# Performance work log

Hardware: AMD Instinct MI355X
Metric: run time of the kernel (lower is better)

The kernel has to match this reference:

```python
import jax, jax.numpy as jnp
import numpy as np

CONTEXT_SIZE = 32
NDIM = 64
HEAD_SIZE = 64
BATCH = 16384


def setup_inputs() -> dict:
    key = jax.random.key(0)
    kx, kk, kq, kv = jax.random.split(key, 4)
    x = jax.random.normal(kx, (BATCH, CONTEXT_SIZE, NDIM), dtype=jnp.float32)
    # nn.Linear(ndim, head_size, bias=False): y = x @ W.T, W is [head_size, ndim].
    # We store transposed weights [ndim, head_size] so y = x @ W.
    scale = 1.0 / np.sqrt(NDIM)
    Wk = jax.random.normal(kk, (NDIM, HEAD_SIZE), dtype=jnp.float32) * scale
    Wq = jax.random.normal(kq, (NDIM, HEAD_SIZE), dtype=jnp.float32) * scale
    Wv = jax.random.normal(kv, (NDIM, HEAD_SIZE), dtype=jnp.float32) * scale
    return {"x": x, "Wk": Wk, "Wq": Wq, "Wv": Wv}


def reference(x, Wk, Wq, Wv):
    # x: [B, T, D] with T == CONTEXT_SIZE
    k = x @ Wk  # [B, T, H]
    q = x @ Wq  # [B, T, H]
    v = x @ Wv  # [B, T, H]
    # Faithful to source: p = q @ k^T / head_size**(-0.5) == q @ k^T * sqrt(head_size)
    p = jnp.einsum("bth,bsh->bts", q, k) * jnp.sqrt(jnp.float32(HEAD_SIZE))
    causal = jnp.tril(jnp.ones((CONTEXT_SIZE, CONTEXT_SIZE), dtype=bool))
    p = jnp.where(causal, p, -jnp.inf)
    p = jax.nn.softmax(p, axis=-1)
    # dropout is identity in eval mode
    return jnp.einsum("bts,bsh->bth", p, v)  # [B, T, H]
```

## Files before the change

### kernel.cpp

```cpp
#include <hip/hip_runtime.h>

typedef __attribute__((ext_vector_type(8))) short short8;
typedef __attribute__((ext_vector_type(4))) float f32x4;
typedef __attribute__((ext_vector_type(2))) unsigned int u32x2;

#define CTX 32
#define ND  64
#define NH  64
#define LOG2E_8 11.541560327111707f

#define OFF_MH 0
#define OFF_ML 8192
#define OFF_WAVE 16384
#define PWSTR 80
#define PW_RTH 0
#define PW_RTL 2560
#define PW_VT  0
#define PW_P   5120
#define WAVE_BYTES 7168
#define NREG 8
#define LDS_BYTES (OFF_WAVE + NREG * WAVE_BYTES)

__device__ __forceinline__ unsigned short f2bf(float f) {
  unsigned int u = __builtin_bit_cast(unsigned int, f);
  u += 0x7FFFu + ((u >> 16) & 1u);
  return (unsigned short)(u >> 16);
}
__device__ __forceinline__ float bf2f(unsigned short b) {
  unsigned int u = ((unsigned int)b) << 16;
  return __builtin_bit_cast(float, u);
}
__device__ __forceinline__ unsigned int pk2(float a, float b) {
  return (unsigned int)f2bf(a) | ((unsigned int)f2bf(b) << 16);
}

#define MFMA(a, b, c) __builtin_amdgcn_mfma_f32_16x16x32_bf16((a), (b), (c), 0, 0, 0)

__global__ __launch_bounds__(256) void mk_m(
    const float* __restrict__ Wq, const float* __restrict__ Wk,
    const float* __restrict__ Wv,
    unsigned short* __restrict__ MtH, unsigned short* __restrict__ MtL,
    unsigned short* __restrict__ WvT)
{
  const int idx = blockIdx.x * 256 + threadIdx.x;
  const int dp = idx >> 6, d = idx & 63;
  const float* wq = Wq + d * 64;
  const float* wk = Wk + dp * 64;
  float acc = 0.f;
  #pragma unroll
  for (int h = 0; h < 64; ++h) acc = fmaf(wq[h], wk[h], acc);
  acc *= LOG2E_8;
  const unsigned short hi = f2bf(acc);
  MtH[idx] = hi;
  MtL[idx] = f2bf(acc - bf2f(hi));
  WvT[idx] = f2bf(Wv[d * 64 + dp]);
}

struct Batch {
  short8 xh[2][2], xl[2][2];
  f32x4  pa[2][2];
  char*  wl;
  float* ob;
};

__device__ __forceinline__ void load_x(const float* __restrict__ xb,
                                       f32x4 (&xr)[2][2][2], int c, int g) {
  #pragma unroll
  for (int mt = 0; mt < 2; ++mt)
    #pragma unroll
    for (int kt = 0; kt < 2; ++kt) {
      const float* p = xb + (16 * mt + c) * ND + 32 * kt + 8 * g;
      xr[mt][kt][0] = *(const f32x4*)(p);
      xr[mt][kt][1] = *(const f32x4*)(p + 4);
    }
}

__device__ __forceinline__ void split_x(Batch& s, const f32x4 (&xr)[2][2][2]) {
  #pragma unroll
  for (int mt = 0; mt < 2; ++mt)
    #pragma unroll
    for (int kt = 0; kt < 2; ++kt) {
      short8 hi, lo;
      #pragma unroll
      for (int half = 0; half < 2; ++half)
        #pragma unroll
        for (int j = 0; j < 4; ++j) {
          const float f = xr[mt][kt][half][j];
          const unsigned short h = f2bf(f);
          hi[4 * half + j] = (short)h;
          lo[4 * half + j] = (short)f2bf(f - bf2f(h));
        }
      s.xh[mt][kt] = hi;
      s.xl[mt][kt] = lo;
    }
  #pragma unroll
  for (int i = 0; i < 2; ++i)
    #pragma unroll
    for (int j = 0; j < 2; ++j) s.pa[i][j] = f32x4{0.f, 0.f, 0.f, 0.f};
}

__device__ __forceinline__ void qk_fill(Batch& s, const char* lds,
                                        int kt, int ntl, int c, int g) {
  const int nt = 2 * kt + ntl;
  f32x4 a0 = {0.f, 0.f, 0.f, 0.f};
  f32x4 a1 = {0.f, 0.f, 0.f, 0.f};
  #pragma unroll
  for (int kk = 0; kk < 2; ++kk) {
    const int row = 16 * nt + c;
    const int byte = row * 128 + ((64 * kk + 16 * g) ^ ((row & 7) << 4));
    const short8 bh = *(const short8*)(lds + OFF_MH + byte);
    const short8 bl = *(const short8*)(lds + OFF_ML + byte);
    a0 = MFMA(s.xh[0][kk], bh, a0);
    a0 = MFMA(s.xh[0][kk], bl, a0);
    a0 = MFMA(s.xl[0][kk], bh, a0);
    a1 = MFMA(s.xh[1][kk], bh, a1);
    a1 = MFMA(s.xh[1][kk], bl, a1);
    a1 = MFMA(s.xl[1][kk], bh, a1);
  }
  #pragma unroll
  for (int j = 0; j < 4; ++j) {
    const int col2 = 2 * (16 * ntl + c);
    const int off0 = (4 * g + j) * PWSTR + col2;
    const int off1 = (16 + 4 * g + j) * PWSTR + col2;
    const unsigned short h0 = f2bf(a0[j]);
    *(unsigned short*)(s.wl + PW_RTH + off0) = h0;
    *(unsigned short*)(s.wl + PW_RTL + off0) = f2bf(a0[j] - bf2f(h0));
    const unsigned short h1 = f2bf(a1[j]);
    *(unsigned short*)(s.wl + PW_RTH + off1) = h1;
    *(unsigned short*)(s.wl + PW_RTL + off1) = f2bf(a1[j] - bf2f(h1));
  }
}

__device__ __forceinline__ void qk_consume(Batch& s, int kt, int c, int g) {
  short8 tH[2], tL[2];
  #pragma unroll
  for (int i = 0; i < 2; ++i) {
    const int off = (16 * i + c) * PWSTR + 16 * g;
    tH[i] = *(const short8*)(s.wl + PW_RTH + off);
    tL[i] = *(const short8*)(s.wl + PW_RTL + off);
  }
  #pragma unroll
  for (int mt = 0; mt < 2; ++mt)
    #pragma unroll
    for (int nt2 = 0; nt2 < 2; ++nt2) {
      s.pa[mt][nt2] = MFMA(s.xh[mt][kt], tH[nt2], s.pa[mt][nt2]);
      s.pa[mt][nt2] = MFMA(s.xl[mt][kt], tH[nt2], s.pa[mt][nt2]);
      s.pa[mt][nt2] = MFMA(s.xh[mt][kt], tL[nt2], s.pa[mt][nt2]);
    }
}

__device__ __forceinline__ void softmax_store(Batch& s, int c, int g) {
  char* const pbuf = s.wl + PW_P;
  #pragma unroll
  for (int nt = 0; nt < 2; ++nt) {
    const int t = 16 * nt + c;
    float v[8];
    #pragma unroll
    for (int mt = 0; mt < 2; ++mt)
      #pragma unroll
      for (int j = 0; j < 4; ++j) {
        const int sidx = 16 * mt + 4 * g + j;
        v[4 * mt + j] = (sidx <= t) ? s.pa[mt][nt][j] : -__builtin_inff();
      }
    float m = fmaxf(fmaxf(fmaxf(v[0], v[1]), fmaxf(v[2], v[3])),
                    fmaxf(fmaxf(v[4], v[5]), fmaxf(v[6], v[7])));
    m = fmaxf(m, __shfl_xor(m, 16));
    m = fmaxf(m, __shfl_xor(m, 32));
    float e[8], ssum = 0.f;
    #pragma unroll
    for (int i = 0; i < 8; ++i) { e[i] = exp2f(v[i] - m); ssum += e[i]; }
    ssum += __shfl_xor(ssum, 16);
    ssum += __shfl_xor(ssum, 32);
    const float r = __builtin_amdgcn_rcpf(ssum);
    #pragma unroll
    for (int mt = 0; mt < 2; ++mt) {
      const u32x2 w2 = {pk2(e[4 * mt] * r, e[4 * mt + 1] * r),
                        pk2(e[4 * mt + 2] * r, e[4 * mt + 3] * r)};
      *(u32x2*)(pbuf + t * 64 + 32 * mt + 8 * g) = w2;
    }
  }
}

__device__ __forceinline__ void vproj(Batch& s, const short8 (&bvr)[4][2],
                                      int c, int g) {
  #pragma unroll
  for (int nt = 0; nt < 4; ++nt) {
    f32x4 a0 = {0.f, 0.f, 0.f, 0.f};
    f32x4 a1 = {0.f, 0.f, 0.f, 0.f};
    #pragma unroll
    for (int kk = 0; kk < 2; ++kk) {
      a0 = MFMA(s.xh[0][kk], bvr[nt][kk], a0);
      a1 = MFMA(s.xh[1][kk], bvr[nt][kk], a1);
    }
    char* const vrow = s.wl + PW_VT + (16 * nt + c) * PWSTR;
    const u32x2 w0 = {pk2(a0[0], a0[1]), pk2(a0[2], a0[3])};
    const u32x2 w1 = {pk2(a1[0], a1[1]), pk2(a1[2], a1[3])};
    *(u32x2*)(vrow + 8 * g)      = w0;
    *(u32x2*)(vrow + 32 + 8 * g) = w1;
  }
}

__device__ __forceinline__ void pv_store(Batch& s, int c, int g) {
  char* const pbuf = s.wl + PW_P;
  const short8 ap0 = *(const short8*)(pbuf + c * 64 + 16 * g);
  const short8 ap1 = *(const short8*)(pbuf + (16 + c) * 64 + 16 * g);
  #pragma unroll
  for (int mh = 0; mh < 4; ++mh) {
    const short8 bv = *(const short8*)(s.wl + PW_VT + (16 * mh + c) * PWSTR + 16 * g);
    f32x4 o0 = {0.f, 0.f, 0.f, 0.f};
    f32x4 o1 = {0.f, 0.f, 0.f, 0.f};
    o0 = MFMA(bv, ap0, o0);
    o1 = MFMA(bv, ap1, o1);
    *(f32x4*)(s.ob + c * NH + 16 * mh + 4 * g)        = o0;
    *(f32x4*)(s.ob + (16 + c) * NH + 16 * mh + 4 * g) = o1;
  }
}

__global__ __launch_bounds__(256, 2) void head_fused(
    const float* __restrict__ x,
    const unsigned short* __restrict__ MtH, const unsigned short* __restrict__ MtL,
    const unsigned short* __restrict__ WvT,
    float* __restrict__ out)
{
  __shared__ __align__(16) char lds[LDS_BYTES];
  const int tid = threadIdx.x;

  {
    const unsigned int* srcH = (const unsigned int*)MtH;
    const unsigned int* srcL = (const unsigned int*)MtL;
    #pragma unroll
    for (int i = 0; i < 8; ++i) {
      const int e = tid + 256 * i;
      const int row = e >> 5;
      const int byte = row * 128 + (((e & 31) * 4) ^ ((row & 7) << 4));
      *(unsigned int*)(lds + OFF_MH + byte) = srcH[e];
      *(unsigned int*)(lds + OFF_ML + byte) = srcL[e];
    }
  }
  __syncthreads();

  const int wid  = tid >> 6;
  const int lane = tid & 63;
  const int c = lane & 15;
  const int g = lane >> 4;

  short8 bvr[4][2];
  #pragma unroll
  for (int nt = 0; nt < 4; ++nt)
    #pragma unroll
    for (int kk = 0; kk < 2; ++kk)
      bvr[nt][kk] = *(const short8*)(WvT + (16 * nt + c) * 64 + 32 * kk + 8 * g);

  const int w = blockIdx.x * 4 + wid;
  const long bA = 2L * w, bB = 2L * w + 1;

  Batch A, B;
  A.wl = lds + OFF_WAVE + (wid * 2 + 0) * WAVE_BYTES;
  B.wl = lds + OFF_WAVE + (wid * 2 + 1) * WAVE_BYTES;
  A.ob = out + bA * (CTX * NH);
  B.ob = out + bB * (CTX * NH);

  f32x4 xrA[2][2][2], xrB[2][2][2];
  load_x(x + bA * (CTX * ND), xrA, c, g);
  load_x(x + bB * (CTX * ND), xrB, c, g);

  split_x(A, xrA);
  split_x(B, xrB);

  #pragma unroll
  for (int kt = 0; kt < 2; ++kt) {
    qk_fill(A, lds, kt, 0, c, g);
    qk_fill(B, lds, kt, 0, c, g);
    qk_fill(A, lds, kt, 1, c, g);
    qk_fill(B, lds, kt, 1, c, g);
    qk_consume(A, kt, c, g);
    qk_consume(B, kt, c, g);
  }
  softmax_store(A, c, g);
  softmax_store(B, c, g);
  vproj(A, bvr, c, g);
  vproj(B, bvr, c, g);
  pv_store(A, c, g);
  pv_store(B, c, g);
}

extern "C" void kernel_launch(void* const* d_in, const int* in_sizes, int n_in,
                              void* d_out, int out_size, void* d_ws, size_t ws_size,
                              hipStream_t stream) {
  const float* x  = (const float*)d_in[0];
  const float* Wk = (const float*)d_in[1];
  const float* Wq = (const float*)d_in[2];
  const float* Wv = (const float*)d_in[3];
  float* out = (float*)d_out;

  unsigned short* MtH = (unsigned short*)d_ws;
  unsigned short* MtL = MtH + 64 * 64;
  unsigned short* WvT = MtL + 64 * 64;

  mk_m<<<dim3(16), dim3(256), 0, stream>>>(Wq, Wk, Wv, MtH, MtL, WvT);

  const int batch = in_sizes[0] / (CTX * ND);
  const int nwg = batch / 8;
  head_fused<<<dim3(nwg), dim3(256), 0, stream>>>(x, MtH, MtL, WvT, out);
}
```

Before: 64.26 us.

## Process batches sequentially per wave with prefetch, packed bf16 conversion, higher occupancy

Each wave now handles its two batches one after another, using a single LDS region, instead of interleaving two batches. The next batch's x is prefetched into registers while the current one is computed. The smaller per-block LDS footprint lets launch bounds ask for three blocks per SIMD. Scalar bf16 rounding is replaced with packed float2-to-bfloat162 conversions, and the P buffer now uses a padded stride. The trade is less instruction-level parallelism from interleaving, in exchange for better occupancy, load latency hiding and cheaper conversions.

Result: faster. 59.64 us (-7.2%).

```diff
diff --git a/kernel.cpp b/kernel.cpp
--- a/kernel.cpp
+++ b/kernel.cpp
@@ -1,13 +1,16 @@
 #include <hip/hip_runtime.h>
+#include <hip/hip_bf16.h>
 
 typedef __attribute__((ext_vector_type(8))) short short8;
 typedef __attribute__((ext_vector_type(4))) float f32x4;
 typedef __attribute__((ext_vector_type(2))) unsigned int u32x2;
+typedef __attribute__((ext_vector_type(4))) unsigned int u32x4;
 
 #define CTX 32
 #define ND  64
 #define NH  64
 #define LOG2E_8 11.541560327111707f
+#define NB_PER_WAVE 2
 
 #define OFF_MH 0
 #define OFF_ML 8192
@@ -17,9 +20,8 @@
 #define PW_RTL 2560
 #define PW_VT  0
 #define PW_P   5120
-#define WAVE_BYTES 7168
-#define NREG 8
-#define LDS_BYTES (OFF_WAVE + NREG * WAVE_BYTES)
+#define WAVE_BYTES 7680
+#define LDS_BYTES (OFF_WAVE + 4 * WAVE_BYTES)
 
 __device__ __forceinline__ unsigned short f2bf(float f) {
   unsigned int u = __builtin_bit_cast(unsigned int, f);
@@ -30,8 +32,16 @@
   unsigned int u = ((unsigned int)b) << 16;
   return __builtin_bit_cast(float, u);
 }
-__device__ __forceinline__ unsigned int pk2(float a, float b) {
-  return (unsigned int)f2bf(a) | ((unsigned int)f2bf(b) << 16);
+__device__ __forceinline__ unsigned int pkrn(float a, float b) {
+  const __hip_bfloat162 t = __float22bfloat162_rn(make_float2(a, b));
+  unsigned int u;
+  __builtin_memcpy(&u, &t, 4);
+  return u;
+}
+__device__ __forceinline__ float2 unpk(unsigned int w) {
+  __hip_bfloat162 t;
+  __builtin_memcpy(&t, &w, 4);
+  return __bfloat1622float2(t);
 }
 
 #define MFMA(a, b, c) __builtin_amdgcn_mfma_f32_16x16x32_bf16((a), (b), (c), 0, 0, 0)
@@ -75,24 +85,36 @@
     }
 }
 
+__device__ __forceinline__ void split8(const f32x4 a0, const f32x4 a1,
+                                       short8& hi, short8& lo) {
+  u32x4 hw, lw;
+  #pragma unroll
+  for (int w = 0; w < 2; ++w) {
+    {
+      const float x0 = a0[2 * w], x1 = a0[2 * w + 1];
+      const unsigned int h = pkrn(x0, x1);
+      const float2 hf = unpk(h);
+      hw[w] = h;
+      lw[w] = pkrn(x0 - hf.x, x1 - hf.y);
+    }
+    {
+      const float x0 = a1[2 * w], x1 = a1[2 * w + 1];
+      const unsigned int h = pkrn(x0, x1);
+      const float2 hf = unpk(h);
+      hw[2 + w] = h;
+      lw[2 + w] = pkrn(x0 - hf.x, x1 - hf.y);
+    }
+  }
+  hi = __builtin_bit_cast(short8, hw);
+  lo = __builtin_bit_cast(short8, lw);
+}
+
 __device__ __forceinline__ void split_x(Batch& s, const f32x4 (&xr)[2][2][2]) {
   #pragma unroll
   for (int mt = 0; mt < 2; ++mt)
     #pragma unroll
-    for (int kt = 0; kt < 2; ++kt) {
-      short8 hi, lo;
-      #pragma unroll
-      for (int half = 0; half < 2; ++half)
-        #pragma unroll
-        for (int j = 0; j < 4; ++j) {
-          const float f = xr[mt][kt][half][j];
-          const unsigned short h = f2bf(f);
-          hi[4 * half + j] = (short)h;
-          lo[4 * half + j] = (short)f2bf(f - bf2f(h));
-        }
-      s.xh[mt][kt] = hi;
-      s.xl[mt][kt] = lo;
-    }
+    for (int kt = 0; kt < 2; ++kt)
+      split8(xr[mt][kt][0], xr[mt][kt][1], s.xh[mt][kt], s.xl[mt][kt]);
   #pragma unroll
   for (int i = 0; i < 2; ++i)
     #pragma unroll
@@ -117,17 +139,29 @@
     a1 = MFMA(s.xh[1][kk], bl, a1);
     a1 = MFMA(s.xl[1][kk], bh, a1);
   }
-  #pragma unroll
-  for (int j = 0; j < 4; ++j) {
-    const int col2 = 2 * (16 * ntl + c);
-    const int off0 = (4 * g + j) * PWSTR + col2;
-    const int off1 = (16 + 4 * g + j) * PWSTR + col2;
-    const unsigned short h0 = f2bf(a0[j]);
-    *(unsigned short*)(s.wl + PW_RTH + off0) = h0;
-    *(unsigned short*)(s.wl + PW_RTL + off0) = f2bf(a0[j] - bf2f(h0));
-    const unsigned short h1 = f2bf(a1[j]);
-    *(unsigned short*)(s.wl + PW_RTH + off1) = h1;
-    *(unsigned short*)(s.wl + PW_RTL + off1) = f2bf(a1[j] - bf2f(h1));
+  const int col2 = 2 * (16 * ntl + c);
+  #pragma unroll
+  for (int pr = 0; pr < 2; ++pr) {
+    {
+      const unsigned int h = pkrn(a0[2 * pr], a0[2 * pr + 1]);
+      const float2 hf = unpk(h);
+      const unsigned int l = pkrn(a0[2 * pr] - hf.x, a0[2 * pr + 1] - hf.y);
+      const int rb = (4 * g + 2 * pr) * PWSTR + col2;
+      *(unsigned short*)(s.wl + PW_RTH + rb)         = (unsigned short)h;
+      *(unsigned short*)(s.wl + PW_RTH + rb + PWSTR) = (unsigned short)(h >> 16);
+      *(unsigned short*)(s.wl + PW_RTL + rb)         = (unsigned short)l;
+      *(unsigned short*)(s.wl + PW_RTL + rb + PWSTR) = (unsigned short)(l >> 16);
+    }
+    {
+      const unsigned int h = pkrn(a1[2 * pr], a1[2 * pr + 1]);
+      const float2 hf = unpk(h);
+      const unsigned int l = pkrn(a1[2 * pr] - hf.x, a1[2 * pr + 1] - hf.y);
+      const int rb = (16 + 4 * g + 2 * pr) * PWSTR + col2;
+      *(unsigned short*)(s.wl + PW_RTH + rb)         = (unsigned short)h;
+      *(unsigned short*)(s.wl + PW_RTH + rb + PWSTR) = (unsigned short)(h >> 16);
+      *(unsigned short*)(s.wl + PW_RTL + rb)         = (unsigned short)l;
+      *(unsigned short*)(s.wl + PW_RTL + rb + PWSTR) = (unsigned short)(l >> 16);
+    }
   }
 }
 
@@ -174,9 +208,9 @@
     const float r = __builtin_amdgcn_rcpf(ssum);
     #pragma unroll
     for (int mt = 0; mt < 2; ++mt) {
-      const u32x2 w2 = {pk2(e[4 * mt] * r, e[4 * mt + 1] * r),
-                        pk2(e[4 * mt + 2] * r, e[4 * mt + 3] * r)};
-      *(u32x2*)(pbuf + t * 64 + 32 * mt + 8 * g) = w2;
+      const u32x2 w2 = {pkrn(e[4 * mt] * r, e[4 * mt + 1] * r),
+                        pkrn(e[4 * mt + 2] * r, e[4 * mt + 3] * r)};
+      *(u32x2*)(pbuf + t * PWSTR + 32 * mt + 8 * g) = w2;
     }
   }
 }
@@ -193,8 +227,8 @@
       a1 = MFMA(s.xh[1][kk], bvr[nt][kk], a1);
     }
     char* const vrow = s.wl + PW_VT + (16 * nt + c) * PWSTR;
-    const u32x2 w0 = {pk2(a0[0], a0[1]), pk2(a0[2], a0[3])};
-    const u32x2 w1 = {pk2(a1[0], a1[1]), pk2(a1[2], a1[3])};
+    const u32x2 w0 = {pkrn(a0[0], a0[1]), pkrn(a0[2], a0[3])};
+    const u32x2 w1 = {pkrn(a1[0], a1[1]), pkrn(a1[2], a1[3])};
     *(u32x2*)(vrow + 8 * g)      = w0;
     *(u32x2*)(vrow + 32 + 8 * g) = w1;
   }
@@ -202,8 +236,8 @@
 
 __device__ __forceinline__ void pv_store(Batch& s, int c, int g) {
   char* const pbuf = s.wl + PW_P;
-  const short8 ap0 = *(const short8*)(pbuf + c * 64 + 16 * g);
-  const short8 ap1 = *(const short8*)(pbuf + (16 + c) * 64 + 16 * g);
+  const short8 ap0 = *(const short8*)(pbuf + c * PWSTR + 16 * g);
+  const short8 ap1 = *(const short8*)(pbuf + (16 + c) * PWSTR + 16 * g);
   #pragma unroll
   for (int mh = 0; mh < 4; ++mh) {
     const short8 bv = *(const short8*)(s.wl + PW_VT + (16 * mh + c) * PWSTR + 16 * g);
@@ -216,11 +250,11 @@
   }
 }
 
-__global__ __launch_bounds__(256, 2) void head_fused(
+__global__ __launch_bounds__(256, 3) void head_fused(
     const float* __restrict__ x,
     const unsigned short* __restrict__ MtH, const unsigned short* __restrict__ MtL,
     const unsigned short* __restrict__ WvT,
-    float* __restrict__ out)
+    float* __restrict__ out, int wstride)
 {
   __shared__ __align__(16) char lds[LDS_BYTES];
   const int tid = threadIdx.x;
@@ -251,37 +285,39 @@
     for (int kk = 0; kk < 2; ++kk)
       bvr[nt][kk] = *(const short8*)(WvT + (16 * nt + c) * 64 + 32 * kk + 8 * g);
 
+  Batch S;
+  S.wl = lds + OFF_WAVE + wid * WAVE_BYTES;
+
   const int w = blockIdx.x * 4 + wid;
-  const long bA = 2L * w, bB = 2L * w + 1;
-
-  Batch A, B;
-  A.wl = lds + OFF_WAVE + (wid * 2 + 0) * WAVE_BYTES;
-  B.wl = lds + OFF_WAVE + (wid * 2 + 1) * WAVE_BYTES;
-  A.ob = out + bA * (CTX * NH);
-  B.ob = out + bB * (CTX * NH);
-
-  f32x4 xrA[2][2][2], xrB[2][2][2];
-  load_x(x + bA * (CTX * ND), xrA, c, g);
-  load_x(x + bB * (CTX * ND), xrB, c, g);
-
-  split_x(A, xrA);
-  split_x(B, xrB);
-
-  #pragma unroll
-  for (int kt = 0; kt < 2; ++kt) {
-    qk_fill(A, lds, kt, 0, c, g);
-    qk_fill(B, lds, kt, 0, c, g);
-    qk_fill(A, lds, kt, 1, c, g);
-    qk_fill(B, lds, kt, 1, c, g);
-    qk_consume(A, kt, c, g);
-    qk_consume(B, kt, c, g);
-  }
-  softmax_store(A, c, g);
-  softmax_store(B, c, g);
-  vproj(A, bvr, c, g);
-  vproj(B, bvr, c, g);
-  pv_store(A, c, g);
-  pv_store(B, c, g);
+
+  f32x4 xc[2][2][2], xn[2][2][2];
+  load_x(x + (long)w * (CTX * ND), xc, c, g);
+
+  #pragma unroll
+  for (int it = 0; it < NB_PER_WAVE; ++it) {
+    const long b = (long)w + (long)it * wstride;
+    if (it + 1 < NB_PER_WAVE)
+      load_x(x + (b + wstride) * (CTX * ND), xn, c, g);
+    S.ob = out + b * (CTX * NH);
+    split_x(S, xc);
+    #pragma unroll
+    for (int kt = 0; kt < 2; ++kt) {
+      qk_fill(S, lds, kt, 0, c, g);
+      qk_fill(S, lds, kt, 1, c, g);
+      qk_consume(S, kt, c, g);
+    }
+    softmax_store(S, c, g);
+    vproj(S, bvr, c, g);
+    pv_store(S, c, g);
+    if (it + 1 < NB_PER_WAVE) {
+      #pragma unroll
+      for (int i = 0; i < 2; ++i)
+        #pragma unroll
+        for (int k = 0; k < 2; ++k)
+          #pragma unroll
+          for (int h = 0; h < 2; ++h) xc[i][k][h] = xn[i][k][h];
+    }
+  }
 }
 
 extern "C" void kernel_launch(void* const* d_in, const int* in_sizes, int n_in,
@@ -300,6 +336,6 @@
   mk_m<<<dim3(16), dim3(256), 0, stream>>>(Wq, Wk, Wv, MtH, MtL, WvT);
 
   const int batch = in_sizes[0] / (CTX * ND);
-  const int nwg = batch / 8;
-  head_fused<<<dim3(nwg), dim3(256), 0, stream>>>(x, MtH, MtL, WvT, out);
-}
+  const int wstride = batch / NB_PER_WAVE;
+  head_fused<<<dim3(wstride / 4), dim3(256), 0, stream>>>(x, MtH, MtL, WvT, out, wstride);
+}
```
